# Performance work log

Hardware: AMD Instinct MI355X
Metric: run time of the kernel (lower is better)

## Reference

```python
import jax, jax.numpy as jnp
import numpy as np
from jax import lax

EMBED = 64
FRAMES = 3
NNB = FRAMES - 1  # neighbor frames


def conv3x3(x, w, b):
    # x: [B,Cin,H,W], w: [Cout,Cin,3,3]
    y = lax.conv_general_dilated(x, w, (1, 1), [(1, 1), (1, 1)],
                                 dimension_numbers=("NCHW", "OIHW", "NCHW"))
    return y + b[None, :, None, None]


def setup_inputs() -> dict:
    key = jax.random.key(0)
    ks = jax.random.split(key, 9)
    s = lambda *sh: 1.0 / np.sqrt(np.prod(sh[1:]))
    return {
        "neighbor_frames": jax.random.normal(ks[0], (2, NNB, 96, 96), jnp.float32),
        "enc_w1": jax.random.normal(ks[1], (EMBED, 1, 3, 3), jnp.float32) * s(EMBED, 1, 3, 3),
        "enc_b1": jnp.zeros((EMBED,), jnp.float32),
        "enc_w2": jax.random.normal(ks[2], (EMBED, EMBED, 3, 3), jnp.float32) * s(EMBED, EMBED, 3, 3),
        "enc_b2": jnp.zeros((EMBED,), jnp.float32),
        "q_w": jax.random.normal(ks[3], (EMBED, NNB * EMBED), jnp.float32) * s(EMBED, NNB * EMBED),
        "q_b": jnp.zeros((EMBED,), jnp.float32),
        "k_w": jax.random.normal(ks[4], (EMBED, NNB * EMBED), jnp.float32) * s(EMBED, NNB * EMBED),
        "k_b": jnp.zeros((EMBED,), jnp.float32),
        "v_w": jax.random.normal(ks[5], (EMBED, NNB * EMBED), jnp.float32) * s(EMBED, NNB * EMBED),
        "v_b": jnp.zeros((EMBED,), jnp.float32),
    }


def reference(neighbor_frames, enc_w1, enc_b1, enc_w2, enc_b2,
              q_w, q_b, k_w, k_b, v_w, v_b):
    B, N, H, W = neighbor_frames.shape
    x = neighbor_frames.reshape(B * N, 1, H, W)
    # conv encoder (3x3 -> relu -> 3x3 -> relu)
    f = jax.nn.relu(conv3x3(x, enc_w1, enc_b1))
    f = jax.nn.relu(conv3x3(f, enc_w2, enc_b2))
    C = f.shape[1]
    # [B,N,C,H,W] -> [B, C*N? no: permute(0,2,1,3,4) -> B, C, N, H, W -> B, C*N, H, W]
    feat = f.reshape(B, N, C, H, W).transpose(0, 2, 1, 3, 4).reshape(B, C * N, H, W)
    # 1x1 qkv convs == per-pixel linear; flatten spatial to tokens t = H*W
    feat_t = feat.reshape(B, C * N, H * W)  # [B, Cin, T]
    Q = jnp.einsum("oc,bct->bot", q_w, feat_t) + q_b[None, :, None]
    K = jnp.einsum("oc,bct->bot", k_w, feat_t) + k_b[None, :, None]
    V = jnp.einsum("oc,bct->bot", v_w, feat_t) + v_b[None, :, None]
    scale = 1.0 / jnp.sqrt(jnp.asarray(Q.shape[1], Q.dtype))
    attn = jnp.einsum("bcn,bcm->bnm", Q, K) * scale  # [B, T, T]
    attn = jax.nn.softmax(attn, axis=-1)
    ctx = jnp.einsum("bnm,bcm->bcn", attn, V)  # [B, C, T]
    return ctx.reshape(B, C, H, W)
```

## Files before the change

### kernel.cpp

```cpp
#include <hip/hip_runtime.h>
#include <hip/hip_bf16.h>

#define TOK 9216
#define KSPLIT 5

typedef _Float16 half8 __attribute__((ext_vector_type(8)));
typedef float f32x4 __attribute__((ext_vector_type(4)));

#define GLOAD_LDS(g, l) \
    __builtin_amdgcn_global_load_lds((const __attribute__((address_space(1))) void*)(g), \
                                     (__attribute__((address_space(3))) void*)(l), 16, 0, 0)

#define QSCALE 0.18033688011112042f

#define OFF_F1   0u
#define SZ_F1    (4u*64u*TOK)
#define OFF_FEAT (OFF_F1 + SZ_F1)
#define SZ_FEAT  (2u*128u*TOK)
#define OFF_Q    (OFF_FEAT + SZ_FEAT)
#define SZ_QKV   (2u*64u*TOK)
#define OFF_K    (OFF_Q + SZ_QKV)
#define OFF_V    (OFF_K + SZ_QKV)
#define OFF_W1   (OFF_V + SZ_QKV)
#define OFF_B1   (OFF_W1 + 576u)
#define OFF_W2T  (OFF_B1 + 64u)
#define OFF_B2   (OFF_W2T + 36864u)
#define OFF_WCAT (OFF_B2 + 64u)
#define OFF_BCAT (OFF_WCAT + 24576u)

#define OFF_QT   OFF_F1
#define OFF_KT   (OFF_F1 + 589824u)
#define OFF_VH   (OFF_F1 + 1179648u)

#define OFF_SLAB0 1769472u
#define OFF_ML2   (OFF_FEAT + 9u*589824u)

__device__ __forceinline__ const float* part_base_c(const float* ws, int slab) {
    return ws + (slab == 0 ? OFF_SLAB0 : (OFF_FEAT + (unsigned)(slab - 1) * 589824u));
}
__device__ __forceinline__ float* part_base(float* ws, int slab) {
    return ws + (slab == 0 ? OFF_SLAB0 : (OFF_FEAT + (unsigned)(slab - 1) * 589824u));
}

__global__ __launch_bounds__(256) void prep_kernel(
    const float* __restrict__ w1, const float* __restrict__ b1,
    const float* __restrict__ w2, const float* __restrict__ b2,
    const float* __restrict__ qw, const float* __restrict__ qb,
    const float* __restrict__ kw, const float* __restrict__ kb,
    const float* __restrict__ vw, const float* __restrict__ vb,
    float* __restrict__ ws)
{
    int gid = blockIdx.x * 256 + threadIdx.x;
    if (gid < 576) ws[OFF_W1 + gid] = w1[gid];
    if (gid < 64) {
        ws[OFF_B1 + gid] = b1[gid];
        ws[OFF_B2 + gid] = b2[gid];
    }
    if (gid < 36864) {
        int co = gid / 576; int rem = gid % 576;
        int ci = rem / 9;  int tp = rem % 9;
        ((_Float16*)(ws + OFF_W2T))[co*576 + tp*64 + ci] = (_Float16)w2[gid];
    }
    if (gid < 24576) {
        int o = gid >> 7; int kidx = gid & 127;
        int n = kidx >> 6, c = kidx & 63;
        int sc = c*2 + n;
        float v;
        if (o < 64)       v = qw[o*128 + sc] * QSCALE;
        else if (o < 128) v = kw[(o-64)*128 + sc];
        else              v = vw[(o-128)*128 + sc];
        ((_Float16*)(ws + OFF_WCAT))[gid] = (_Float16)v;
    }
    if (gid < 192) {
        float v;
        if (gid < 64)       v = qb[gid] * QSCALE;
        else if (gid < 128) v = kb[gid-64];
        else                v = vb[gid-128];
        ws[OFF_BCAT + gid] = v;
    }
}

__global__ __launch_bounds__(256) void conv1_kernel(
    const float* __restrict__ x, float* __restrict__ ws)
{
    const float* w1f = ws + OFF_W1;
    const float* b1f = ws + OFF_B1;
    _Float16* f1h = (_Float16*)(ws + OFF_F1);
    int gid = blockIdx.x * 256 + threadIdx.x;
    int img = gid / TOK;
    int p   = gid % TOK;
    int h = p / 96, w = p % 96;
    float xv[9];
    #pragma unroll
    for (int dh = 0; dh < 3; ++dh)
        #pragma unroll
        for (int dw = 0; dw < 3; ++dw) {
            int r = h + dh - 1, c = w + dw - 1;
            bool ok = (r >= 0) && (r < 96) && (c >= 0) && (c < 96);
            xv[dh*3 + dw] = ok ? x[img*TOK + r*96 + c] : 0.f;
        }
    _Float16* dst = f1h + (size_t)gid * 64;
    #pragma unroll
    for (int g8 = 0; g8 < 8; ++g8) {
        union { _Float16 h[8]; uint4 u; } pk8;
        #pragma unroll
        for (int j = 0; j < 8; ++j) {
            int co = g8*8 + j;
            float a = b1f[co];
            #pragma unroll
            for (int t = 0; t < 9; ++t) a += w1f[co*9 + t] * xv[t];
            pk8.h[j] = (_Float16)fmaxf(a, 0.f);
        }
        *(uint4*)&dst[g8*8] = pk8.u;
    }
}

__global__ __launch_bounds__(256) void conv2_kernel(float* __restrict__ ws)
{
    int bid = blockIdx.x;
    int img = bid & 3;
    int tile = bid >> 2;
    int tid = threadIdx.x;
    int lane = tid & 63, w = tid >> 6;
    int lr = lane & 15, lk = lane >> 4;

    const _Float16* f1h = (const _Float16*)(ws + OFF_F1) + (size_t)img*TOK*64;
    const _Float16* Wc  = (const _Float16*)(ws + OFF_W2T);
    const float* b2f = ws + OFF_B2;

    int t = tile*64 + w*16 + lr;
    int h = t / 96, wc = t % 96;

    half8 z8;
    #pragma unroll
    for (int i = 0; i < 8; ++i) z8[i] = (_Float16)0.f;

    f32x4 acc[4];
    #pragma unroll
    for (int cs = 0; cs < 4; ++cs) {
        float bv = b2f[cs*16 + lr];
        acc[cs] = (f32x4){bv, bv, bv, bv};
    }

    #pragma unroll
    for (int ch = 0; ch < 18; ++ch) {
        int k = ch*32 + lk*8;
        int tap = k >> 6, ci = k & 63;
        int dh = tap / 3, dw = tap % 3;
        int r = h + dh - 1, c = wc + dw - 1;
        half8 af = z8;
        if ((unsigned)r < 96u && (unsigned)c < 96u)
            af = *(const half8*)&f1h[(size_t)(r*96 + c)*64 + ci];
        #pragma unroll
        for (int cs = 0; cs < 4; ++cs) {
            half8 bfr = *(const half8*)&Wc[(size_t)(cs*16 + lr)*576 + k];
            acc[cs] = __builtin_amdgcn_mfma_f32_16x16x32_f16(af, bfr, acc[cs], 0, 0, 0);
        }
    }

    _Float16* featH2 = (_Float16*)(ws + OFF_FEAT) + (size_t)img*TOK*64;
    int tbase = tile*64 + w*16 + 4*lk;
    #pragma unroll
    for (int cs = 0; cs < 4; ++cs)
        #pragma unroll
        for (int r = 0; r < 4; ++r)
            featH2[(size_t)(tbase + r)*64 + cs*16 + lr] = (_Float16)fmaxf(acc[cs][r], 0.f);
}

__global__ __launch_bounds__(256) void qkvgemm_kernel(float* __restrict__ ws)
{
    int bid = blockIdx.x;
    int b   = bid / 288;
    int tt0 = (bid % 288) * 32;
    int tid = threadIdx.x;
    int lane = tid & 63, w = tid >> 6;
    int lr = lane & 15, lk = lane >> 4;

    const _Float16* fH = (const _Float16*)(ws + OFF_FEAT) + (size_t)b*2*TOK*64;
    const _Float16* W  = (const _Float16*)(ws + OFF_WCAT);
    const float* bc = ws + OFF_BCAT;
    _Float16* QT = (_Float16*)(ws + OFF_QT) + (size_t)b*TOK*64;
    _Float16* KT = (_Float16*)(ws + OFF_KT) + (size_t)b*TOK*64;
    _Float16* VH = (_Float16*)(ws + OFF_VH) + (size_t)b*64*TOK;

    half8 bf[2][4];
    #pragma unroll
    for (int tt = 0; tt < 2; ++tt)
        #pragma unroll
        for (int kc = 0; kc < 4; ++kc) {
            int k = kc*32 + lk*8;
            bf[tt][kc] = *(const half8*)&fH[(size_t)(k >> 6)*TOK*64
                                            + (size_t)(tt0 + tt*16 + lr)*64 + (k & 63)];
        }

    half8 af[3][4];
    #pragma unroll
    for (int i = 0; i < 3; ++i)
        #pragma unroll
        for (int kc = 0; kc < 4; ++kc)
            af[i][kc] = *(const half8*)&W[(size_t)((w*3 + i)*16 + lr)*128 + kc*32 + lk*8];

    #pragma unroll
    for (int i = 0; i < 3; ++i) {
        int ot = w*3 + i;
        f32x4 a0, a1;
        #pragma unroll
        for (int r = 0; r < 4; ++r) {
            float bv = bc[ot*16 + 4*lk + r];
            a0[r] = bv; a1[r] = bv;
        }
        #pragma unroll
        for (int kc = 0; kc < 4; ++kc) {
            a0 = __builtin_amdgcn_mfma_f32_16x16x32_f16(af[i][kc], bf[0][kc], a0, 0, 0, 0);
            a1 = __builtin_amdgcn_mfma_f32_16x16x32_f16(af[i][kc], bf[1][kc], a1, 0, 0, 0);
        }
        #pragma unroll
        for (int tt = 0; tt < 2; ++tt) {
            f32x4 a = tt ? a1 : a0;
            int t = tt0 + tt*16 + lr;
            if (ot < 4) {
                union { _Float16 h[4]; uint2 u; } p;
                #pragma unroll
                for (int r = 0; r < 4; ++r) p.h[r] = (_Float16)a[r];
                *(uint2*)&QT[(size_t)t*64 + ot*16 + 4*lk] = p.u;
            } else if (ot < 8) {
                union { _Float16 h[4]; uint2 u; } p;
                #pragma unroll
                for (int r = 0; r < 4; ++r) p.h[r] = (_Float16)a[r];
                *(uint2*)&KT[(size_t)t*64 + (ot-4)*16 + 4*lk] = p.u;
            } else {
                #pragma unroll
                for (int r = 0; r < 4; ++r)
                    VH[(size_t)((ot-8)*16 + 4*lk + r)*TOK + t] = (_Float16)a[r];
            }
        }
    }
}

__global__ __launch_bounds__(256, 8) void attn_kernel(float* __restrict__ ws)
{
    __shared__ __align__(16) char smem[17408];
    float* ldsf = (float*)smem;

    int bid = blockIdx.x;
    int b   = bid / (144*KSPLIT);
    int rem = bid % (144*KSPLIT);
    int qt  = rem / KSPLIT;
    int ks  = rem % KSPLIT;
    int tid = threadIdx.x;
    int lane = tid & 63, w = tid >> 6;
    int q0 = qt * 64;
    int lr = lane & 15;
    int lk = lane >> 4;

    int kb0 = (ks*288)/KSPLIT, kb1 = ((ks+1)*288)/KSPLIT;
    int nit = kb1 - kb0;
    int slab = b*KSPLIT + ks;

    const _Float16* Qt = (const _Float16*)(ws + OFF_QT) + (size_t)b*TOK*64;
    const _Float16* Kt = (const _Float16*)(ws + OFF_KT) + (size_t)b*TOK*64;
    const _Float16* Vh = (const _Float16*)(ws + OFF_VH) + (size_t)b*64*TOK;
    float* part = part_base(ws, slab);
    float* ml   = ws + OFF_ML2 + (size_t)slab*2*TOK;

    half8 qB[2];
    #pragma unroll
    for (int ch = 0; ch < 2; ++ch)
        qB[ch] = *(const half8*)&Qt[(size_t)(q0 + w*16 + lr)*64 + ch*32 + lk*8];

    const f32x4 Z4 = (f32x4){0.f, 0.f, 0.f, 0.f};
    half8 ones;
    #pragma unroll
    for (int i = 0; i < 8; ++i) ones[i] = (_Float16)1.0f;

    f32x4 O[4];
    #pragma unroll
    for (int cs = 0; cs < 4; ++cs) O[cs] = Z4;
    f32x4 lacc = Z4;
    float mM = -INFINITY;

    int ksegl = ((lane & 7) ^ ((lane >> 3) & 7)) * 8;
    int vsegl = ((lane & 3) ^ ((lane >> 2) & 3)) * 8;
    unsigned kOff = (unsigned)(kb0*32 + w*8 + (lane >> 3))*64u + (unsigned)ksegl;
    unsigned vOff = (unsigned)(w*16 + (lane >> 2))*(unsigned)TOK
                    + (unsigned)(kb0*32) + (unsigned)vsegl;
    unsigned wbase = (unsigned)(w * 1024);

    GLOAD_LDS(Kt + kOff, smem +        wbase);
    GLOAD_LDS(Vh + vOff, smem + 8192 + wbase);
    asm volatile("s_waitcnt vmcnt(0)" ::: "memory");
    __builtin_amdgcn_s_barrier();

    for (int it = 0; it < nit; ++it) {
        char* sKb = smem +        (it & 1) * 4096;
        char* sVb = smem + 8192 + (it & 1) * 4096;

        if (it + 1 < nit) {
            unsigned kN = kOff + (unsigned)(it + 1) * 2048u;
            unsigned vN = vOff + (unsigned)(it + 1) * 32u;
            GLOAD_LDS(Kt + kN, smem +        ((it + 1) & 1) * 4096 + wbase);
            GLOAD_LDS(Vh + vN, smem + 8192 + ((it + 1) & 1) * 4096 + wbase);
        }

        f32x4 S[2];
        __builtin_amdgcn_s_setprio(1);
        #pragma unroll
        for (int st = 0; st < 2; ++st) {
            int t = st*16 + lr;
            half8 kA0 = *(const half8*)(sKb + ((t*128 +      lk*16) ^ ((t&7)<<4)));
            half8 kA1 = *(const half8*)(sKb + ((t*128 + 64 + lk*16) ^ ((t&7)<<4)));
            f32x4 s = __builtin_amdgcn_mfma_f32_16x16x32_f16(kA0, qB[0], Z4, 0, 0, 0);
            S[st]   = __builtin_amdgcn_mfma_f32_16x16x32_f16(kA1, qB[1], s,  0, 0, 0);
        }
        __builtin_amdgcn_s_setprio(0);

        float m0 = fmaxf(fmaxf(S[0][0], S[0][1]), fmaxf(S[0][2], S[0][3]));
        float m1 = fmaxf(fmaxf(S[1][0], S[1][1]), fmaxf(S[1][2], S[1][3]));
        float pm = fmaxf(m0, m1);
        pm = fmaxf(pm, __shfl_xor(pm, 16));
        pm = fmaxf(pm, __shfl_xor(pm, 32));

        if (__any(pm > mM + 8.0f)) {
            float mn = fmaxf(mM, pm);
            float fs = exp2f(mM - mn);
            mM = mn;
            #pragma unroll
            for (int cs = 0; cs < 4; ++cs)
                #pragma unroll
                for (int r = 0; r < 4; ++r) O[cs][r] *= fs;
            #pragma unroll
            for (int r = 0; r < 4; ++r) lacc[r] *= fs;
        }

        #pragma unroll
        for (int st = 0; st < 2; ++st)
            #pragma unroll
            for (int r = 0; r < 4; ++r)
                S[st][r] = exp2f(S[st][r] - mM);

        unsigned int pk2[2][2];
        #pragma unroll
        for (int st = 0; st < 2; ++st) {
            pk2[st][0] = __builtin_bit_cast(unsigned int,
                             __builtin_amdgcn_cvt_pkrtz(S[st][0], S[st][1]));
            pk2[st][1] = __builtin_bit_cast(unsigned int,
                             __builtin_amdgcn_cvt_pkrtz(S[st][2], S[st][3]));
        }

        int srcA = lr + 32*(lk & 1);
        int sel  = lk >> 1;
        union { unsigned int u[4]; half8 h; } pb;
        #pragma unroll
        for (int w2 = 0; w2 < 4; ++w2) {
            int src = srcA + 16*(w2 >> 1);
            int lo = __shfl((int)pk2[0][w2 & 1], src);
            int hi = __shfl((int)pk2[1][w2 & 1], src);
            pb.u[w2] = (unsigned int)(sel ? hi : lo);
        }

        __builtin_amdgcn_s_setprio(1);
        lacc = __builtin_amdgcn_mfma_f32_16x16x32_f16(ones, pb.h, lacc, 0, 0, 0);
        #pragma unroll
        for (int cs = 0; cs < 4; ++cs) {
            int crow = cs*16 + lr;
            half8 vA = *(const half8*)(sVb + ((crow*64 + lk*16) ^ ((crow&3)<<4)));
            O[cs] = __builtin_amdgcn_mfma_f32_16x16x32_f16(vA, pb.h, O[cs], 0, 0, 0);
        }
        __builtin_amdgcn_s_setprio(0);

        asm volatile("s_waitcnt vmcnt(0)" ::: "memory");
        __builtin_amdgcn_s_barrier();
    }

    if (lk == 0) {
        ml[q0 + w*16 + lr]       = mM;
        ml[TOK + q0 + w*16 + lr] = lacc[0];
    }

    #pragma unroll
    for (int cs = 0; cs < 4; ++cs)
        #pragma unroll
        for (int r = 0; r < 4; ++r)
            ldsf[(cs*16 + 4*lk + r)*68 + w*16 + lr] = O[cs][r];
    __syncthreads();
    int c = tid >> 2, sg = tid & 3;
    const float* srcr = &ldsf[c*68 + sg*16];
    float* dstr = &part[(size_t)c*TOK + q0 + sg*16];
    #pragma unroll
    for (int j = 0; j < 4; ++j)
        *(float4*)&dstr[j*4] = *(const float4*)&srcr[j*4];
}

__global__ __launch_bounds__(256) void recombine_kernel(
    const float* __restrict__ ws, float* __restrict__ out)
{
    int gid = blockIdx.x * 256 + threadIdx.x;
    int b   = gid / (4*TOK);
    int rem = gid % (4*TOK);
    int cg  = rem / TOK;
    int t   = rem % TOK;
    const float* mlp = ws + OFF_ML2;

    float m[KSPLIT], l[KSPLIT];
    float M = -INFINITY;
    #pragma unroll
    for (int ks = 0; ks < KSPLIT; ++ks) {
        int slab = b*KSPLIT + ks;
        m[ks] = mlp[(size_t)slab*2*TOK + t];
        l[ks] = mlp[(size_t)slab*2*TOK + TOK + t];
        M = fmaxf(M, m[ks]);
    }
    float wgt[KSPLIT];
    float denom = 0.f;
    #pragma unroll
    for (int ks = 0; ks < KSPLIT; ++ks) {
        wgt[ks] = exp2f(m[ks] - M);
        denom += l[ks] * wgt[ks];
    }
    float inv = 1.f / denom;
    #pragma unroll
    for (int cc = 0; cc < 16; ++cc) {
        int c = cg*16 + cc;
        float acc = 0.f;
        #pragma unroll
        for (int ks = 0; ks < KSPLIT; ++ks) {
            const float* part = part_base_c(ws, b*KSPLIT + ks);
            acc += part[(size_t)c*TOK + t] * wgt[ks];
        }
        out[(size_t)(b*64 + c)*TOK + t] = acc * inv;
    }
}

extern "C" void kernel_launch(void* const* d_in, const int* in_sizes, int n_in,
                              void* d_out, int out_size, void* d_ws, size_t ws_size,
                              hipStream_t stream)
{
    const float* frames = (const float*)d_in[0];
    const float* w1 = (const float*)d_in[1];
    const float* b1 = (const float*)d_in[2];
    const float* w2 = (const float*)d_in[3];
    const float* b2 = (const float*)d_in[4];
    const float* qw = (const float*)d_in[5];
    const float* qb = (const float*)d_in[6];
    const float* kw = (const float*)d_in[7];
    const float* kb = (const float*)d_in[8];
    const float* vw = (const float*)d_in[9];
    const float* vb = (const float*)d_in[10];
    float* ws = (float*)d_ws;
    float* out = (float*)d_out;

    hipLaunchKernelGGL(prep_kernel, dim3(144), dim3(256), 0, stream,
                       w1, b1, w2, b2, qw, qb, kw, kb, vw, vb, ws);
    hipLaunchKernelGGL(conv1_kernel, dim3(144), dim3(256), 0, stream, frames, ws);
    hipLaunchKernelGGL(conv2_kernel, dim3(576), dim3(256), 0, stream, ws);
    hipLaunchKernelGGL(qkvgemm_kernel, dim3(576), dim3(256), 0, stream, ws);
    hipLaunchKernelGGL(attn_kernel, dim3(2*144*KSPLIT), dim3(256), 0, stream, ws);
    hipLaunchKernelGGL(recombine_kernel, dim3(288), dim3(256), 0, stream, ws, out);
}
```

Measured before the change: 174.3 us.

## Widen attention blocks to 128 queries, fuse prep into conv1, vectorize recombine

The attention kernel now runs 512-thread blocks covering 128 query rows. Each K/V tile staged in LDS is shared by eight waves instead of four, with waves 0-3 loading K and waves 4-7 loading V, which halves global K/V traffic per query. The weight-prep kernel is merged into conv1, which now reads w1/b1 directly, removing one launch. Recombine processes four tokens per thread using float4 loads and stores. The trade-offs are fewer, larger attention blocks (720 instead of 1440), possible register or occupancy limits at 512 threads, and an extra LDS round trip with barriers for the output write-back.

After: 170.0 us. 1.03x faster.

```diff
diff --git a/kernel.cpp b/kernel.cpp
--- a/kernel.cpp
+++ b/kernel.cpp
@@ -17,11 +17,7 @@
 #define SZ_F1    (4u*64u*TOK)
 #define OFF_FEAT (OFF_F1 + SZ_F1)
 #define SZ_FEAT  (2u*128u*TOK)
-#define OFF_Q    (OFF_FEAT + SZ_FEAT)
-#define SZ_QKV   (2u*64u*TOK)
-#define OFF_K    (OFF_Q + SZ_QKV)
-#define OFF_V    (OFF_K + SZ_QKV)
-#define OFF_W1   (OFF_V + SZ_QKV)
+#define OFF_W1   (OFF_FEAT + SZ_FEAT + 3u*2u*64u*TOK)
 #define OFF_B1   (OFF_W1 + 576u)
 #define OFF_W2T  (OFF_B1 + 64u)
 #define OFF_B2   (OFF_W2T + 36864u)
@@ -42,7 +38,8 @@
     return ws + (slab == 0 ? OFF_SLAB0 : (OFF_FEAT + (unsigned)(slab - 1) * 589824u));
 }
 
-__global__ __launch_bounds__(256) void prep_kernel(
+__global__ __launch_bounds__(256) void conv1_kernel(
+    const float* __restrict__ x,
     const float* __restrict__ w1, const float* __restrict__ b1,
     const float* __restrict__ w2, const float* __restrict__ b2,
     const float* __restrict__ qw, const float* __restrict__ qb,
@@ -51,11 +48,8 @@
     float* __restrict__ ws)
 {
     int gid = blockIdx.x * 256 + threadIdx.x;
-    if (gid < 576) ws[OFF_W1 + gid] = w1[gid];
-    if (gid < 64) {
-        ws[OFF_B1 + gid] = b1[gid];
-        ws[OFF_B2 + gid] = b2[gid];
-    }
+
+    if (gid < 64) ws[OFF_B2 + gid] = b2[gid];
     if (gid < 36864) {
         int co = gid / 576; int rem = gid % 576;
         int ci = rem / 9;  int tp = rem % 9;
@@ -78,15 +72,8 @@
         else                v = vb[gid-128];
         ws[OFF_BCAT + gid] = v;
     }
-}
-
-__global__ __launch_bounds__(256) void conv1_kernel(
-    const float* __restrict__ x, float* __restrict__ ws)
-{
-    const float* w1f = ws + OFF_W1;
-    const float* b1f = ws + OFF_B1;
+
     _Float16* f1h = (_Float16*)(ws + OFF_F1);
-    int gid = blockIdx.x * 256 + threadIdx.x;
     int img = gid / TOK;
     int p   = gid % TOK;
     int h = p / 96, w = p % 96;
@@ -106,9 +93,9 @@
         #pragma unroll
         for (int j = 0; j < 8; ++j) {
             int co = g8*8 + j;
-            float a = b1f[co];
+            float a = b1[co];
             #pragma unroll
-            for (int t = 0; t < 9; ++t) a += w1f[co*9 + t] * xv[t];
+            for (int t = 0; t < 9; ++t) a += w1[co*9 + t] * xv[t];
             pk8.h[j] = (_Float16)fmaxf(a, 0.f);
         }
         *(uint4*)&dst[g8*8] = pk8.u;
@@ -237,19 +224,19 @@
     }
 }
 
-__global__ __launch_bounds__(256, 8) void attn_kernel(float* __restrict__ ws)
+__global__ __launch_bounds__(512, 8) void attn_kernel(float* __restrict__ ws)
 {
     __shared__ __align__(16) char smem[17408];
     float* ldsf = (float*)smem;
 
     int bid = blockIdx.x;
-    int b   = bid / (144*KSPLIT);
-    int rem = bid % (144*KSPLIT);
+    int b   = bid / (72*KSPLIT);
+    int rem = bid % (72*KSPLIT);
     int qt  = rem / KSPLIT;
     int ks  = rem % KSPLIT;
     int tid = threadIdx.x;
     int lane = tid & 63, w = tid >> 6;
-    int q0 = qt * 64;
+    int q0 = qt * 128;
     int lr = lane & 15;
     int lk = lane >> 4;
 
@@ -281,13 +268,14 @@
 
     int ksegl = ((lane & 7) ^ ((lane >> 3) & 7)) * 8;
     int vsegl = ((lane & 3) ^ ((lane >> 2) & 3)) * 8;
-    unsigned kOff = (unsigned)(kb0*32 + w*8 + (lane >> 3))*64u + (unsigned)ksegl;
-    unsigned vOff = (unsigned)(w*16 + (lane >> 2))*(unsigned)TOK
+    int wq = w & 3;
+    unsigned kOff = (unsigned)(kb0*32 + wq*8 + (lane >> 3))*64u + (unsigned)ksegl;
+    unsigned vOff = (unsigned)(wq*16 + (lane >> 2))*(unsigned)TOK
                     + (unsigned)(kb0*32) + (unsigned)vsegl;
-    unsigned wbase = (unsigned)(w * 1024);
-
-    GLOAD_LDS(Kt + kOff, smem +        wbase);
-    GLOAD_LDS(Vh + vOff, smem + 8192 + wbase);
+    unsigned wbase = (unsigned)(wq * 1024);
+
+    if (w < 4) GLOAD_LDS(Kt + kOff, smem + wbase);
+    else       GLOAD_LDS(Vh + vOff, smem + 8192 + wbase);
     asm volatile("s_waitcnt vmcnt(0)" ::: "memory");
     __builtin_amdgcn_s_barrier();
 
@@ -296,10 +284,9 @@
         char* sVb = smem + 8192 + (it & 1) * 4096;
 
         if (it + 1 < nit) {
-            unsigned kN = kOff + (unsigned)(it + 1) * 2048u;
-            unsigned vN = vOff + (unsigned)(it + 1) * 32u;
-            GLOAD_LDS(Kt + kN, smem +        ((it + 1) & 1) * 4096 + wbase);
-            GLOAD_LDS(Vh + vN, smem + 8192 + ((it + 1) & 1) * 4096 + wbase);
+            unsigned bufo = (unsigned)(((it + 1) & 1) * 4096) + wbase;
+            if (w < 4) GLOAD_LDS(Kt + kOff + (unsigned)(it + 1) * 2048u, smem + bufo);
+            else       GLOAD_LDS(Vh + vOff + (unsigned)(it + 1) * 32u,   smem + 8192 + bufo);
         }
 
         f32x4 S[2];
@@ -378,56 +365,67 @@
     }
 
     #pragma unroll
-    for (int cs = 0; cs < 4; ++cs)
-        #pragma unroll
-        for (int r = 0; r < 4; ++r)
-            ldsf[(cs*16 + 4*lk + r)*68 + w*16 + lr] = O[cs][r];
-    __syncthreads();
-    int c = tid >> 2, sg = tid & 3;
-    const float* srcr = &ldsf[c*68 + sg*16];
-    float* dstr = &part[(size_t)c*TOK + q0 + sg*16];
-    #pragma unroll
-    for (int j = 0; j < 4; ++j)
-        *(float4*)&dstr[j*4] = *(const float4*)&srcr[j*4];
+    for (int h = 0; h < 2; ++h) {
+        if ((w >> 2) == h) {
+            #pragma unroll
+            for (int cs = 0; cs < 4; ++cs)
+                #pragma unroll
+                for (int r = 0; r < 4; ++r)
+                    ldsf[(cs*16 + 4*lk + r)*68 + wq*16 + lr] = O[cs][r];
+        }
+        __syncthreads();
+        int c = tid >> 3, qs = (tid & 7) * 8;
+        const float* srcr = &ldsf[c*68 + qs];
+        float* dstr = &part[(size_t)c*TOK + q0 + h*64 + qs];
+        *(float4*)&dstr[0] = *(const float4*)&srcr[0];
+        *(float4*)&dstr[4] = *(const float4*)&srcr[4];
+        __syncthreads();
+    }
 }
 
 __global__ __launch_bounds__(256) void recombine_kernel(
     const float* __restrict__ ws, float* __restrict__ out)
 {
     int gid = blockIdx.x * 256 + threadIdx.x;
-    int b   = gid / (4*TOK);
-    int rem = gid % (4*TOK);
-    int cg  = rem / TOK;
-    int t   = rem % TOK;
+    int b   = gid / 9216;
+    int rem = gid % 9216;
+    int cg  = rem / 2304;
+    int t   = (rem % 2304) * 4;
     const float* mlp = ws + OFF_ML2;
 
-    float m[KSPLIT], l[KSPLIT];
-    float M = -INFINITY;
+    float4 m4[KSPLIT], l4[KSPLIT];
+    float4 M = {-INFINITY, -INFINITY, -INFINITY, -INFINITY};
     #pragma unroll
     for (int ks = 0; ks < KSPLIT; ++ks) {
         int slab = b*KSPLIT + ks;
-        m[ks] = mlp[(size_t)slab*2*TOK + t];
-        l[ks] = mlp[(size_t)slab*2*TOK + TOK + t];
-        M = fmaxf(M, m[ks]);
-    }
-    float wgt[KSPLIT];
-    float denom = 0.f;
+        m4[ks] = *(const float4*)&mlp[(size_t)slab*2*TOK + t];
+        l4[ks] = *(const float4*)&mlp[(size_t)slab*2*TOK + TOK + t];
+        M.x = fmaxf(M.x, m4[ks].x); M.y = fmaxf(M.y, m4[ks].y);
+        M.z = fmaxf(M.z, m4[ks].z); M.w = fmaxf(M.w, m4[ks].w);
+    }
+    float4 wgt[KSPLIT];
+    float4 den = {0.f, 0.f, 0.f, 0.f};
     #pragma unroll
     for (int ks = 0; ks < KSPLIT; ++ks) {
-        wgt[ks] = exp2f(m[ks] - M);
-        denom += l[ks] * wgt[ks];
-    }
-    float inv = 1.f / denom;
+        wgt[ks].x = exp2f(m4[ks].x - M.x); wgt[ks].y = exp2f(m4[ks].y - M.y);
+        wgt[ks].z = exp2f(m4[ks].z - M.z); wgt[ks].w = exp2f(m4[ks].w - M.w);
+        den.x += l4[ks].x * wgt[ks].x; den.y += l4[ks].y * wgt[ks].y;
+        den.z += l4[ks].z * wgt[ks].z; den.w += l4[ks].w * wgt[ks].w;
+    }
+    float4 inv = {1.f/den.x, 1.f/den.y, 1.f/den.z, 1.f/den.w};
     #pragma unroll
     for (int cc = 0; cc < 16; ++cc) {
         int c = cg*16 + cc;
-        float acc = 0.f;
+        float4 acc = {0.f, 0.f, 0.f, 0.f};
         #pragma unroll
         for (int ks = 0; ks < KSPLIT; ++ks) {
             const float* part = part_base_c(ws, b*KSPLIT + ks);
-            acc += part[(size_t)c*TOK + t] * wgt[ks];
-        }
-        out[(size_t)(b*64 + c)*TOK + t] = acc * inv;
+            float4 p4 = *(const float4*)&part[(size_t)c*TOK + t];
+            acc.x += p4.x * wgt[ks].x; acc.y += p4.y * wgt[ks].y;
+            acc.z += p4.z * wgt[ks].z; acc.w += p4.w * wgt[ks].w;
+        }
+        float4 o4 = {acc.x*inv.x, acc.y*inv.y, acc.z*inv.z, acc.w*inv.w};
+        *(float4*)&out[(size_t)(b*64 + c)*TOK + t] = o4;
     }
 }
 
@@ -449,11 +447,10 @@
     float* ws = (float*)d_ws;
     float* out = (float*)d_out;
 
-    hipLaunchKernelGGL(prep_kernel, dim3(144), dim3(256), 0, stream,
-                       w1, b1, w2, b2, qw, qb, kw, kb, vw, vb, ws);
-    hipLaunchKernelGGL(conv1_kernel, dim3(144), dim3(256), 0, stream, frames, ws);
+    hipLaunchKernelGGL(conv1_kernel, dim3(144), dim3(256), 0, stream,
+                       frames, w1, b1, w2, b2, qw, qb, kw, kb, vw, vb, ws);
     hipLaunchKernelGGL(conv2_kernel, dim3(576), dim3(256), 0, stream, ws);
     hipLaunchKernelGGL(qkvgemm_kernel, dim3(576), dim3(256), 0, stream, ws);
-    hipLaunchKernelGGL(attn_kernel, dim3(2*144*KSPLIT), dim3(256), 0, stream, ws);
-    hipLaunchKernelGGL(recombine_kernel, dim3(288), dim3(256), 0, stream, ws, out);
-}
+    hipLaunchKernelGGL(attn_kernel, dim3(2*72*KSPLIT), dim3(512), 0, stream, ws);
+    hipLaunchKernelGGL(recombine_kernel, dim3(72), dim3(256), 0, stream, ws, out);
+}
```
